# Performance work log

Measured on AMD Instinct MI355X. Metric: run time of the kernel, lower is better.

## Reference

```python
import jax, jax.numpy as jnp
import numpy as np

B, L, N_IN, N_STATE = 32, 4096, 8, 8
C_IN, C_OUT = N_IN + N_STATE, N_STATE
H, M, N_LAYERS = 64, 64, 4


def setup_inputs() -> dict:
    key = jax.random.key(0)
    ks = jax.random.split(key, 16)
    s = 0.02
    return {
        "u": jax.random.normal(ks[0], (B, L, N_IN), jnp.float32),
        "z": jax.random.normal(ks[1], (B, N_STATE), jnp.float32),
        "t": jax.random.uniform(ks[2], (B, 1), jnp.float32),
        "w_lift": jax.random.normal(ks[3], (H, C_IN), jnp.float32) * s,
        "b_lift": jnp.zeros((H,), jnp.float32),
        "spec_wr": jax.random.normal(ks[4], (N_LAYERS, H, H, M), jnp.float32) / (H),
        "spec_wi": jax.random.normal(ks[5], (N_LAYERS, H, H, M), jnp.float32) / (H),
        "w_skip": jax.random.normal(ks[6], (N_LAYERS, H, H), jnp.float32) * s,
        "b_skip": jnp.zeros((N_LAYERS, H), jnp.float32),
        "w_p1": jax.random.normal(ks[7], (2 * H, H), jnp.float32) * s,
        "b_p1": jnp.zeros((2 * H,), jnp.float32),
        "w_p2": jax.random.normal(ks[8], (C_OUT, 2 * H), jnp.float32) * s,
        "b_p2": jnp.zeros((C_OUT,), jnp.float32),
    }


def _fno_forward(u, z, w_lift, b_lift, spec_wr, spec_wi, w_skip, b_skip, w_p1, b_p1, w_p2, b_p2):
    b, l, _ = u.shape
    rep_z = jnp.broadcast_to(z[:, None, :], (b, l, z.shape[1]))
    x = jnp.concatenate([u, rep_z], axis=-1)          # [B, L, C_in]
    x = jnp.transpose(x, (0, 2, 1))                   # [B, C_in, L]
    # lifting (1x1 conv)
    x = jnp.einsum("bcl,hc->bhl", x, w_lift) + b_lift[None, :, None]
    n_layers, _, _, m = spec_wr.shape
    for i in range(n_layers):
        xf = jnp.fft.rfft(x, axis=-1)                 # [B, H, L//2+1] complex
        w = spec_wr[i] + 1j * spec_wi[i]              # [H, H, M]
        of = jnp.einsum("bim,oim->bom", xf[..., :m], w)
        of = jnp.pad(of, ((0, 0), (0, 0), (0, xf.shape[-1] - m)))
        xs = jnp.fft.irfft(of, n=l, axis=-1)          # [B, H, L]
        sk = jnp.einsum("bil,oi->bol", x, w_skip[i]) + b_skip[i][None, :, None]
        x = xs + sk
        if i < n_layers - 1:
            x = jax.nn.gelu(x)
    # projection: H -> 2H -> C_out (1x1 convs)
    x = jax.nn.gelu(jnp.einsum("bhl,ph->bpl", x, w_p1) + b_p1[None, :, None])
    x = jnp.einsum("bpl,op->bol", x, w_p2) + b_p2[None, :, None]
    outs = jnp.transpose(x, (0, 2, 1))                # [B, L, C_out]
    return outs[:, -1, :]                             # [B, C_out]


def reference(u, z, t, w_lift, b_lift, spec_wr, spec_wi, w_skip, b_skip, w_p1, b_p1, w_p2, b_p2):
    # t is accepted by the original forward but unused in FNOProjection
    return _fno_forward(u, z, w_lift, b_lift, spec_wr, spec_wi, w_skip, b_skip, w_p1, b_p1, w_p2, b_p2)
```

## Files before the change

kernel.cpp:

```cpp
#include <hip/hip_runtime.h>
#include <math.h>

typedef _Float16 f16;
typedef f16  f16x2 __attribute__((ext_vector_type(2)));
typedef f16  f16x4 __attribute__((ext_vector_type(4)));
typedef f16  f16x8 __attribute__((ext_vector_type(8)));
typedef float f32x4 __attribute__((ext_vector_type(4)));

#define F4(p)  (*(float4*)(p))
#define CF4(p) (*(const float4*)(p))

namespace {
constexpr int LL = 4096;
constexpr int HH = 64;

__device__ __forceinline__ float gelu_fast(float x) {
    float inner = 0.7978845608028654f * (x + 0.044715f * x * x * x);
    float e = __expf(-2.0f * inner);
    return x / (1.0f + e);
}

__device__ __forceinline__ f32x4 mfma16(f16x8 a, f16x8 b, f32x4 c) {
    return __builtin_amdgcn_mfma_f32_16x16x32_f16(a, b, c, 0, 0, 0);
}
}

__global__ __launch_bounds__(256) void k_init(const float* __restrict__ u,
                                              const float* __restrict__ z,
                                              const float* __restrict__ wl,
                                              const float* __restrict__ bl,
                                              const float* __restrict__ wsk,
                                              const float* __restrict__ wr,
                                              const float* __restrict__ wi,
                                              f16* __restrict__ Tdt,
                                              f16* __restrict__ Ttr,
                                              f16* __restrict__ wskh,
                                              f16* __restrict__ wrh,
                                              f16* __restrict__ wih,
                                              f16* __restrict__ XT0) {
    const int bid = blockIdx.x;
    const int t = threadIdx.x;
    if (bid < 512) {
        const int b = bid >> 4;
        const int l0 = (bid & 15) * 256;
        constexpr int IP = 260;
        __shared__ float in_s[16 * IP];
        __shared__ float wsh[64 * 16];
        __shared__ float bsh[64];
        for (int i = t; i < 1024; i += 256) wsh[i] = wl[i];
        if (t < 64) bsh[t] = bl[t];
#pragma unroll
        for (int q = 0; q < 2; ++q) {
            int f = t + q * 256;
            int l = f >> 1, cq = (f & 1) * 4;
            float4 v = CF4(u + ((size_t)b * LL + l0 + l) * 8 + cq);
            in_s[(cq + 0) * IP + l] = v.x;
            in_s[(cq + 1) * IP + l] = v.y;
            in_s[(cq + 2) * IP + l] = v.z;
            in_s[(cq + 3) * IP + l] = v.w;
        }
        for (int f = t; f < 8 * 256; f += 256) {
            int c = f >> 8, l = f & 255;
            in_s[(8 + c) * IP + l] = z[b * 8 + c];
        }
        __syncthreads();
        const int hg = t >> 5, lsub = t & 31;
        float acc[8][8] = {};
        for (int c = 0; c < 16; ++c) {
            float wv[8], inv[8];
#pragma unroll
            for (int i = 0; i < 8; ++i) wv[i] = wsh[(hg * 8 + i) * 16 + c];
#pragma unroll
            for (int j = 0; j < 8; ++j) inv[j] = in_s[c * IP + lsub + 32 * j];
#pragma unroll
            for (int i = 0; i < 8; ++i)
#pragma unroll
                for (int j = 0; j < 8; ++j) acc[i][j] += wv[i] * inv[j];
        }
#pragma unroll
        for (int j = 0; j < 8; ++j) {
            __attribute__((aligned(16))) f16 hv[8];
#pragma unroll
            for (int i = 0; i < 8; ++i) hv[i] = (f16)(acc[i][j] + bsh[hg * 8 + i]);
            int l = l0 + lsub + 32 * j;
            F4(XT0 + ((size_t)b * LL + l) * HH + hg * 8) = CF4(hv);
        }
    } else if (bid < 1536) {
        const int tb = bid - 512;
        const float w0 = 6.283185307179586f / 4096.0f;
        {
            int m = tb >> 4;
            int l = ((tb & 15) << 8) + t;
            float s, c;
            sincosf((float)((l * m) & 4095) * w0, &s, &c);
            Tdt[(size_t)(2 * m) * LL + l]     = (f16)c;
            Tdt[(size_t)(2 * m + 1) * LL + l] = (f16)(-s);
        }
        {
            int l = tb * 4 + (t >> 6);
            int m = t & 63;
            float s, c;
            sincosf((float)((l * m) & 4095) * w0, &s, &c);
            const float sc = 1.0f / 4096.0f;
            f16x2 pv;
            pv.x = (f16)((m == 0) ? sc : 2.0f * sc * c);
            pv.y = (f16)((m == 0) ? 0.0f : -2.0f * sc * s);
            *(f16x2*)(Ttr + (size_t)l * 128 + 2 * m) = pv;
        }
        if (tb < 64) {
            int idx = tb * 256 + t;
            wskh[idx] = (f16)wsk[idx];
        }
    } else {
        const int cb = bid - 1536;
        size_t base = (size_t)cb * 1024 + t * 4;
        float4 vr = CF4(wr + base);
        float4 vi = CF4(wi + base);
        f16x4 hr, hi;
        hr.x = (f16)vr.x; hr.y = (f16)vr.y; hr.z = (f16)vr.z; hr.w = (f16)vr.w;
        hi.x = (f16)vi.x; hi.y = (f16)vi.y; hi.z = (f16)vi.z; hi.w = (f16)vi.w;
        *(f16x4*)(wrh + base) = hr;
        *(f16x4*)(wih + base) = hi;
    }
}

__global__ __launch_bounds__(256) void k_dft(const f16* __restrict__ XT,
                                             const f16* __restrict__ Tdt,
                                             f16* __restrict__ Y) {
    __shared__ f16 Asl[32 * 72];
    __shared__ f16 Bsl[128 * 72];
    const int t = threadIdx.x;
    const int ch = blockIdx.x >> 1, h0 = (blockIdx.x & 1) * 32, b = blockIdx.y;
    const int lane = t & 63, wid = t >> 6;
    const int mh = (wid & 1) * 16, n0 = (wid >> 1) * 64;
    const int fm = lane & 15, fq = lane >> 4;
    f32x4 acc[4] = {};
    for (int k0 = 0; k0 < 512; k0 += 64) {
        const int l0 = ch * 512 + k0;
        __syncthreads();
        {
            int seg = t >> 6;
            f16x8 v = *(const f16x8*)(XT + ((size_t)b * LL + l0 + lane) * HH + h0 + seg * 8);
#pragma unroll
            for (int i = 0; i < 8; ++i) Asl[(seg * 8 + i) * 72 + lane] = v[i];
        }
#pragma unroll
        for (int p = 0; p < 4; ++p) {
            int r = (t >> 3) + p * 32;
            F4(&Bsl[r * 72 + (t & 7) * 8]) = CF4(Tdt + (size_t)r * LL + l0 + (t & 7) * 8);
        }
        __syncthreads();
#pragma unroll
        for (int ks = 0; ks < 64; ks += 32) {
            f16x8 a = *(const f16x8*)&Asl[(mh + fm) * 72 + ks + fq * 8];
#pragma unroll
            for (int j = 0; j < 4; ++j) {
                f16x8 bj = *(const f16x8*)&Bsl[(n0 + j * 16 + fm) * 72 + ks + fq * 8];
                acc[j] = mfma16(a, bj, acc[j]);
            }
        }
    }
    f16* yp = Y + ((size_t)ch * 2048 + b * HH + h0) * 128;
#pragma unroll
    for (int j = 0; j < 4; ++j)
#pragma unroll
        for (int r = 0; r < 4; ++r)
            yp[(size_t)(mh + fq * 4 + r) * 128 + n0 + j * 16 + fm] = (f16)acc[j][r];
}

__global__ __launch_bounds__(256) void k_spec(const f16* __restrict__ Y,
                                              const f16* __restrict__ wrh,
                                              const f16* __restrict__ wih,
                                              f16* __restrict__ Ofh, int layer) {
    __shared__ float xsh[64 * 128];
    const int t = threadIdx.x;
    const int b = blockIdx.x;
    const int og = blockIdx.y;
    {
#pragma unroll
        for (int i = 0; i < 4; ++i) {
            int g = t + i * 256;
            float s[8] = {};
#pragma unroll
            for (int c = 0; c < 8; ++c) {
                f16x8 v = *(const f16x8*)(Y + ((size_t)c * 2048 + b * HH) * 128 + g * 8);
#pragma unroll
                for (int e = 0; e < 8; ++e) s[e] += (float)v[e];
            }
#pragma unroll
            for (int e = 0; e < 8; ++e) xsh[g * 8 + e] = s[e];
        }
    }
    __syncthreads();
    const int m = t & 63, osub = t >> 6;
    const int o = og * 4 + osub;
    const f16* wrp = wrh + ((size_t)layer * HH + o) * HH * 64 + m;
    const f16* wip = wih + ((size_t)layer * HH + o) * HH * 64 + m;
    float are = 0.0f, aim = 0.0f;
    const float2* xs2 = (const float2*)xsh;
#pragma unroll 8
    for (int i = 0; i < 64; ++i) {
        float2 xv = xs2[i * 64 + m];
        float wrv = (float)wrp[(size_t)i * 64];
        float wiv = (float)wip[(size_t)i * 64];
        are += xv.x * wrv - xv.y * wiv;
        aim += xv.x * wiv + xv.y * wrv;
    }
    f16x2 ov; ov.x = (f16)are; ov.y = (f16)aim;
    *(f16x2*)(Ofh + ((size_t)b * HH + o) * 128 + 2 * m) = ov;
}

__global__ __launch_bounds__(256) void k_recon(const f16* __restrict__ Ofh,
                                               const f16* __restrict__ XT,
                                               const f16* __restrict__ Ttr,
                                               const f16* __restrict__ wskh,
                                               const float* __restrict__ bsk,
                                               f16* __restrict__ XTn,
                                               int layer) {
    __shared__ f16 Asl[64 * 200];
    __shared__ f16 Bsl[128 * 72];
    const int t = threadIdx.x;
    const int l0 = blockIdx.x * 128, b = blockIdx.y;
    const int lane = t & 63, wid = t >> 6;
    const int m0 = (wid & 1) * 32, n0 = (wid >> 1) * 64;
    const int fm = lane & 15, fq = lane >> 4;
    f32x4 acc[2][4] = {};
    {
        int seg = t & 15, row = t >> 4;
#pragma unroll
        for (int p = 0; p < 4; ++p) {
            int r = row + p * 16;
            F4(&Asl[r * 200 + seg * 8]) = CF4(Ofh + ((size_t)(b * HH + r)) * 128 + seg * 8);
        }
        int seg8 = t & 7, row8 = t >> 3;
#pragma unroll
        for (int p = 0; p < 2; ++p) {
            int r = row8 + p * 32;
            F4(&Asl[r * 200 + 128 + seg8 * 8]) =
                CF4(wskh + ((size_t)(layer * HH + r)) * HH + seg8 * 8);
        }
    }
    const int srow = t >> 3, sseg = t & 7;
    for (int k0 = 0; k0 < 192; k0 += 64) {
        __syncthreads();
#pragma unroll
        for (int p = 0; p < 4; ++p) {
            int r = srow + p * 32;
            const f16* src = (k0 < 128)
                ? (Ttr + (size_t)(l0 + r) * 128 + k0 + sseg * 8)
                : (XT + ((size_t)b * LL + l0 + r) * HH + sseg * 8);
            F4(&Bsl[r * 72 + sseg * 8]) = CF4(src);
        }
        __syncthreads();
#pragma unroll
        for (int ks = 0; ks < 64; ks += 32) {
            f16x8 a0 = *(const f16x8*)&Asl[(m0 + fm) * 200 + k0 + ks + fq * 8];
            f16x8 a1 = *(const f16x8*)&Asl[(m0 + 16 + fm) * 200 + k0 + ks + fq * 8];
#pragma unroll
            for (int j = 0; j < 4; ++j) {
                f16x8 bj = *(const f16x8*)&Bsl[(n0 + j * 16 + fm) * 72 + ks + fq * 8];
                acc[0][j] = mfma16(a0, bj, acc[0][j]);
                acc[1][j] = mfma16(a1, bj, acc[1][j]);
            }
        }
    }
    __syncthreads();
#pragma unroll
    for (int i = 0; i < 2; ++i)
#pragma unroll
        for (int r = 0; r < 4; ++r) {
            int row = m0 + i * 16 + fq * 4 + r;
            float bias = bsk[layer * HH + row];
#pragma unroll
            for (int j = 0; j < 4; ++j) {
                float v = gelu_fast(acc[i][j][r] + bias);
                int lc = n0 + j * 16 + fm;
                Bsl[lc * 72 + row] = (f16)v;
            }
        }
    __syncthreads();
    {
        int row = t >> 1, half = t & 1;
        f16* dst = XTn + ((size_t)b * LL + l0 + row) * HH + half * 32;
        const f16* src = &Bsl[row * 72 + half * 32];
#pragma unroll
        for (int i = 0; i < 4; ++i)
            F4(dst + i * 8) = CF4(src + i * 8);
    }
}

__global__ __launch_bounds__(128) void k_final(const f16* __restrict__ Ofh,
                                               const f16* __restrict__ XT3,
                                               const f16* __restrict__ Ttr,
                                               const float* __restrict__ wsk,
                                               const float* __restrict__ bsk,
                                               const float* __restrict__ wp1,
                                               const float* __restrict__ bp1,
                                               const float* __restrict__ wp2,
                                               const float* __restrict__ bp2,
                                               float* __restrict__ out) {
    __shared__ float ofs[64 * 129];
    __shared__ float wsks[64 * 65];
    __shared__ float wp1s[128 * 65];
    __shared__ float tl[128], xl[64], x4[64], y[128];
    const int b = blockIdx.x, t = threadIdx.x;
    {
#pragma unroll
        for (int i = 0; i < 8; ++i) {
            int g = t + i * 128;
            f16x8 v = *(const f16x8*)(Ofh + (size_t)b * HH * 128 + g * 8);
            int o = g >> 4, k0 = (g & 15) * 8;
#pragma unroll
            for (int e = 0; e < 8; ++e) ofs[o * 129 + k0 + e] = (float)v[e];
        }
    }
    {
        const float* src = wsk + 3 * HH * HH;
#pragma unroll
        for (int i = 0; i < 8; ++i) {
            int g = t + i * 128;
            float4 v = CF4(src + g * 4);
            int o = g >> 4, c0 = (g & 15) * 4;
            F4(&wsks[o * 65 + c0]) = v;
        }
    }
    {
#pragma unroll
        for (int i = 0; i < 16; ++i) {
            int g = t + i * 128;
            float4 v = CF4(wp1 + g * 4);
            int p = g >> 4, c0 = (g & 15) * 4;
            F4(&wp1s[p * 65 + c0]) = v;
        }
    }
    tl[t] = (float)Ttr[(size_t)(LL - 1) * 128 + t];
    if (t < 64) xl[t] = (float)XT3[((size_t)b * LL + (LL - 1)) * HH + t];
    __syncthreads();
    if (t < 64) {
        const int o = t;
        float acc = bsk[3 * HH + o];
        for (int k = 0; k < 128; ++k) acc += ofs[o * 129 + k] * tl[k];
        for (int i = 0; i < 64; ++i) acc += wsks[o * 65 + i] * xl[i];
        x4[o] = acc;
    }
    __syncthreads();
    {
        float acc = bp1[t];
        for (int h = 0; h < 64; ++h) acc += wp1s[t * 65 + h] * x4[h];
        y[t] = gelu_fast(acc);
    }
    __syncthreads();
    if (t < 8) {
        float acc = bp2[t];
        for (int p = 0; p < 128; ++p) acc += wp2[t * 128 + p] * y[p];
        out[b * 8 + t] = acc;
    }
}

extern "C" void kernel_launch(void* const* d_in, const int* in_sizes, int n_in,
                              void* d_out, int out_size, void* d_ws, size_t ws_size,
                              hipStream_t stream) {
    (void)in_sizes; (void)n_in; (void)out_size; (void)ws_size;
    const float* u   = (const float*)d_in[0];
    const float* z   = (const float*)d_in[1];
    const float* wl  = (const float*)d_in[3];
    const float* bl  = (const float*)d_in[4];
    const float* swr = (const float*)d_in[5];
    const float* swi = (const float*)d_in[6];
    const float* wsk = (const float*)d_in[7];
    const float* bsk = (const float*)d_in[8];
    const float* wp1 = (const float*)d_in[9];
    const float* bp1 = (const float*)d_in[10];
    const float* wp2 = (const float*)d_in[11];
    const float* bp2 = (const float*)d_in[12];
    float* out = (float*)d_out;

    f16* ws    = (f16*)d_ws;
    f16* XTa   = ws;
    f16* XTb   = XTa + 8388608;
    f16* Tdt   = XTb + 8388608;
    f16* Ttr   = Tdt + 524288;
    f16* Ofh   = Ttr + 524288;
    f16* wskh  = Ofh + 262144;
    f16* wrh   = wskh + 16384;
    f16* wih   = wrh + 1048576;

    k_init<<<2560, 256, 0, stream>>>(u, z, wl, bl, wsk, swr, swi,
                                     Tdt, Ttr, wskh, wrh, wih, XTa);

    f16* xtc = XTa; f16* xtn = XTb;
    for (int layer = 0; layer < 4; ++layer) {
        f16* Y = xtn;
        k_dft<<<dim3(16, 32), 256, 0, stream>>>(xtc, Tdt, Y);
        k_spec<<<dim3(32, 16), 256, 0, stream>>>(Y, wrh, wih, Ofh, layer);
        if (layer < 3) {
            k_recon<<<dim3(32, 32), 256, 0, stream>>>(Ofh, xtc, Ttr, wskh, bsk,
                                                      xtn, layer);
            f16* tmp = xtc; xtc = xtn; xtn = tmp;
        } else {
            k_final<<<32, 128, 0, stream>>>(Ofh, xtc, Ttr, wsk, bsk,
                                            wp1, bp1, wp2, bp2, out);
        }
    }
}
```

Baseline: 211.7 us.

## Fuse layer reconstruction with next layer's forward DFT into one kernel

Replaces the separate recon and DFT kernels with a fused kernel. Each block reconstructs four 128-wide L chunks of the new activation, applies GELU, and immediately accumulates the truncated forward DFT of those chunks into per-block partial Y sums. This removes a launch per layer and avoids re-reading the activation for the DFT. On layer 2 it skips writing the full activation and stores only the last position, which is all k_final needs. In exchange, the DFT now runs over only 8 L-blocks per batch, so the partial Y (8 slices) must be reduced downstream, presumably by k_spec, which this code does not show changing. The fused kernel also uses fewer, larger blocks and more shared memory.

```diff
diff --git a/kernel.cpp b/kernel.cpp
--- a/kernel.cpp
+++ b/kernel.cpp
@@ -210,83 +210,125 @@
     *(f16x2*)(Ofh + ((size_t)b * HH + o) * 128 + 2 * m) = ov;
 }
 
-__global__ __launch_bounds__(256) void k_recon(const f16* __restrict__ Ofh,
-                                               const f16* __restrict__ XT,
-                                               const f16* __restrict__ Ttr,
-                                               const f16* __restrict__ wskh,
-                                               const float* __restrict__ bsk,
-                                               f16* __restrict__ XTn,
-                                               int layer) {
+__global__ __launch_bounds__(512, 4) void k_fused(const f16* __restrict__ Ofh,
+                                                  const f16* __restrict__ XTold,
+                                                  const f16* __restrict__ Ttr,
+                                                  const f16* __restrict__ wskh,
+                                                  const float* __restrict__ bsk,
+                                                  const f16* __restrict__ Tdt,
+                                                  f16* __restrict__ XTn,
+                                                  f16* __restrict__ Y,
+                                                  int layer) {
+    __shared__ f16 XA[64 * 136];
     __shared__ f16 Asl[64 * 200];
     __shared__ f16 Bsl[128 * 72];
+    __shared__ float bss[64];
     const int t = threadIdx.x;
-    const int l0 = blockIdx.x * 128, b = blockIdx.y;
+    const int lc = blockIdx.x, b = blockIdx.y;
     const int lane = t & 63, wid = t >> 6;
-    const int m0 = (wid & 1) * 32, n0 = (wid >> 1) * 64;
+    const int ow = (wid & 1) * 32;
+    const int n0 = (wid >> 1) * 32;
     const int fm = lane & 15, fq = lane >> 4;
-    f32x4 acc[2][4] = {};
     {
         int seg = t & 15, row = t >> 4;
 #pragma unroll
-        for (int p = 0; p < 4; ++p) {
-            int r = row + p * 16;
+        for (int p = 0; p < 2; ++p) {
+            int r = row + p * 32;
             F4(&Asl[r * 200 + seg * 8]) = CF4(Ofh + ((size_t)(b * HH + r)) * 128 + seg * 8);
         }
-        int seg8 = t & 7, row8 = t >> 3;
-#pragma unroll
-        for (int p = 0; p < 2; ++p) {
-            int r = row8 + p * 32;
-            F4(&Asl[r * 200 + 128 + seg8 * 8]) =
-                CF4(wskh + ((size_t)(layer * HH + r)) * HH + seg8 * 8);
-        }
-    }
-    const int srow = t >> 3, sseg = t & 7;
-    for (int k0 = 0; k0 < 192; k0 += 64) {
-        __syncthreads();
-#pragma unroll
-        for (int p = 0; p < 4; ++p) {
-            int r = srow + p * 32;
-            const f16* src = (k0 < 128)
-                ? (Ttr + (size_t)(l0 + r) * 128 + k0 + sseg * 8)
-                : (XT + ((size_t)b * LL + l0 + r) * HH + sseg * 8);
-            F4(&Bsl[r * 72 + sseg * 8]) = CF4(src);
-        }
-        __syncthreads();
-#pragma unroll
-        for (int ks = 0; ks < 64; ks += 32) {
-            f16x8 a0 = *(const f16x8*)&Asl[(m0 + fm) * 200 + k0 + ks + fq * 8];
-            f16x8 a1 = *(const f16x8*)&Asl[(m0 + 16 + fm) * 200 + k0 + ks + fq * 8];
-#pragma unroll
-            for (int j = 0; j < 4; ++j) {
-                f16x8 bj = *(const f16x8*)&Bsl[(n0 + j * 16 + fm) * 72 + ks + fq * 8];
-                acc[0][j] = mfma16(a0, bj, acc[0][j]);
-                acc[1][j] = mfma16(a1, bj, acc[1][j]);
-            }
-        }
-    }
-    __syncthreads();
+        int sg8 = t & 7, r8 = t >> 3;
+        F4(&Asl[r8 * 200 + 128 + sg8 * 8]) =
+            CF4(wskh + ((size_t)(layer * HH + r8)) * HH + sg8 * 8);
+        if (t < 64) bss[t] = bsk[layer * HH + t];
+    }
+    f32x4 Yac[2][2] = {};
+    for (int ls = 0; ls < 4; ++ls) {
+        const int l0g = lc * 512 + ls * 128;
+        f32x4 acc[2][2] = {};
+#pragma unroll
+        for (int k0 = 0; k0 < 192; k0 += 64) {
+            __syncthreads();
+#pragma unroll
+            for (int p = 0; p < 2; ++p) {
+                int item = t + p * 512;
+                int r = item >> 3, sg = item & 7;
+                const f16* src = (k0 < 128)
+                    ? (Ttr + (size_t)(l0g + r) * 128 + k0 + sg * 8)
+                    : (XTold + ((size_t)b * LL + l0g + r) * HH + sg * 8);
+                F4(&Bsl[r * 72 + sg * 8]) = CF4(src);
+            }
+            __syncthreads();
+#pragma unroll
+            for (int ks = 0; ks < 64; ks += 32) {
+                f16x8 a0 = *(const f16x8*)&Asl[(ow + fm) * 200 + k0 + ks + fq * 8];
+                f16x8 a1 = *(const f16x8*)&Asl[(ow + 16 + fm) * 200 + k0 + ks + fq * 8];
+#pragma unroll
+                for (int j = 0; j < 2; ++j) {
+                    f16x8 bj = *(const f16x8*)&Bsl[(n0 + j * 16 + fm) * 72 + ks + fq * 8];
+                    acc[0][j] = mfma16(a0, bj, acc[0][j]);
+                    acc[1][j] = mfma16(a1, bj, acc[1][j]);
+                }
+            }
+        }
+        __syncthreads();
+#pragma unroll
+        for (int i = 0; i < 2; ++i)
+#pragma unroll
+            for (int r = 0; r < 4; ++r) {
+                int row = ow + i * 16 + fq * 4 + r;
+                float bias = bss[row];
+#pragma unroll
+                for (int j = 0; j < 2; ++j) {
+                    int lcn = n0 + j * 16 + fm;
+                    f16 hv = (f16)gelu_fast(acc[i][j][r] + bias);
+                    XA[row * 136 + lcn] = hv;
+                    Bsl[lcn * 72 + row] = hv;
+                }
+            }
+        __syncthreads();
+        if (layer < 2) {
+#pragma unroll
+            for (int p = 0; p < 2; ++p) {
+                int item = t + p * 512;
+                int r = item >> 3, sg = item & 7;
+                F4(XTn + ((size_t)b * LL + l0g + r) * HH + sg * 8) = CF4(&Bsl[r * 72 + sg * 8]);
+            }
+        } else if (lc == 7 && ls == 3) {
+            if (t < 64) XTn[((size_t)b * LL + (LL - 1)) * HH + t] = Bsl[127 * 72 + t];
+        }
+        __syncthreads();
+#pragma unroll
+        for (int c = 0; c < 2; ++c) {
+            if (c) __syncthreads();
+#pragma unroll
+            for (int p = 0; p < 2; ++p) {
+                int item = t + p * 512;
+                int r = item >> 3, sg = item & 7;
+                F4(&Bsl[r * 72 + sg * 8]) = CF4(Tdt + (size_t)r * LL + l0g + c * 64 + sg * 8);
+            }
+            __syncthreads();
+#pragma unroll
+            for (int ks = 0; ks < 64; ks += 32) {
+                f16x8 a0 = *(const f16x8*)&XA[(ow + fm) * 136 + c * 64 + ks + fq * 8];
+                f16x8 a1 = *(const f16x8*)&XA[(ow + 16 + fm) * 136 + c * 64 + ks + fq * 8];
+#pragma unroll
+                for (int j = 0; j < 2; ++j) {
+                    f16x8 bj = *(const f16x8*)&Bsl[(n0 + j * 16 + fm) * 72 + ks + fq * 8];
+                    Yac[0][j] = mfma16(a0, bj, Yac[0][j]);
+                    Yac[1][j] = mfma16(a1, bj, Yac[1][j]);
+                }
+            }
+        }
+    }
+    f16* yp = Y + ((size_t)lc * 2048 + (size_t)b * HH) * 128;
 #pragma unroll
     for (int i = 0; i < 2; ++i)
 #pragma unroll
-        for (int r = 0; r < 4; ++r) {
-            int row = m0 + i * 16 + fq * 4 + r;
-            float bias = bsk[layer * HH + row];
-#pragma unroll
-            for (int j = 0; j < 4; ++j) {
-                float v = gelu_fast(acc[i][j][r] + bias);
-                int lc = n0 + j * 16 + fm;
-                Bsl[lc * 72 + row] = (f16)v;
-            }
-        }
-    __syncthreads();
-    {
-        int row = t >> 1, half = t & 1;
-        f16* dst = XTn + ((size_t)b * LL + l0 + row) * HH + half * 32;
-        const f16* src = &Bsl[row * 72 + half * 32];
-#pragma unroll
-        for (int i = 0; i < 4; ++i)
-            F4(dst + i * 8) = CF4(src + i * 8);
-    }
+        for (int j = 0; j < 2; ++j)
+#pragma unroll
+            for (int r = 0; r < 4; ++r)
+                yp[(size_t)(ow + i * 16 + fq * 4 + r) * 128 + n0 + j * 16 + fm] =
+                    (f16)Yac[i][j][r];
 }
 
 __global__ __launch_bounds__(128) void k_final(const f16* __restrict__ Ofh,
@@ -384,18 +426,19 @@
     f16* wskh  = Ofh + 262144;
     f16* wrh   = wskh + 16384;
     f16* wih   = wrh + 1048576;
+    f16* Yb    = wih + 1048576;
 
     k_init<<<2560, 256, 0, stream>>>(u, z, wl, bl, wsk, swr, swi,
                                      Tdt, Ttr, wskh, wrh, wih, XTa);
 
+    k_dft<<<dim3(16, 32), 256, 0, stream>>>(XTa, Tdt, Yb);
+
     f16* xtc = XTa; f16* xtn = XTb;
     for (int layer = 0; layer < 4; ++layer) {
-        f16* Y = xtn;
-        k_dft<<<dim3(16, 32), 256, 0, stream>>>(xtc, Tdt, Y);
-        k_spec<<<dim3(32, 16), 256, 0, stream>>>(Y, wrh, wih, Ofh, layer);
+        k_spec<<<dim3(32, 16), 256, 0, stream>>>(Yb, wrh, wih, Ofh, layer);
         if (layer < 3) {
-            k_recon<<<dim3(32, 32), 256, 0, stream>>>(Ofh, xtc, Ttr, wskh, bsk,
-                                                      xtn, layer);
+            k_fused<<<dim3(8, 32), 512, 0, stream>>>(Ofh, xtc, Ttr, wskh, bsk,
+                                                     Tdt, xtn, Yb, layer);
             f16* tmp = xtc; xtc = xtn; xtn = tmp;
         } else {
             k_final<<<32, 128, 0, stream>>>(Ofh, xtc, Ttr, wsk, bsk,
```

Result: slower. 218.2 us (+3.1%).
